# Performance work log

Measured on AMD Instinct MI355X. Metric: run time of the kernel, lower is better.

## Reference

```python
import jax, jax.numpy as jnp
import numpy as np

C, G = 512, 16            # channels, groups
GC = C // G               # group channels = 32
OFFSET_SCALE = 1.0
EPS = 1e-6


def setup_inputs() -> dict:
    key = jax.random.key(0)
    ks = jax.random.split(key, 4)
    N, H, W = 8, 64, 64
    return {
        "input_first": jax.random.normal(ks[0], (N, C, H, W), jnp.float32),
        "input_last": jax.random.normal(ks[1], (N, H, W, C), jnp.float32),
        "dw_w": jax.random.normal(ks[2], (C, 1, 3, 3), jnp.float32) * 0.1,  # depthwise kernel (OIHW, I=1)
        "dw_b": jnp.zeros((C,), jnp.float32),
        "ln_g": jnp.ones((C,), jnp.float32),
        "ln_b": jnp.zeros((C,), jnp.float32),
        "off_w": jax.random.normal(ks[3], (2 * G, C), jnp.float32) * 0.02,  # nonzero (module zero-inits)
        "off_b": jnp.zeros((2 * G,), jnp.float32),
    }


def _bilinear(img, px, py):
    # align_corners=False, padding_mode='zeros'.
    Hin, Win, _ = img.shape
    x0 = jnp.floor(px)
    y0 = jnp.floor(py)
    wx1 = px - x0
    wy1 = py - y0

    def tap(xi, yi, w):
        xc = jnp.clip(xi, 0, Win - 1).astype(jnp.int32)
        yc = jnp.clip(yi, 0, Hin - 1).astype(jnp.int32)
        valid = ((xi >= 0) & (xi <= Win - 1) & (yi >= 0) & (yi <= Hin - 1)).astype(img.dtype)
        return img[yc, xc] * (w * valid)[:, None]  # [L, GC]

    return (tap(x0, y0, (1 - wx1) * (1 - wy1)) + tap(x0 + 1, y0, wx1 * (1 - wy1)) +
            tap(x0, y0 + 1, (1 - wx1) * wy1) + tap(x0 + 1, y0 + 1, wx1 * wy1))


_sampler = jax.vmap(jax.vmap(_bilinear))  # over [N, G, ...]


def _forward(input_first, input_last, dw_w, dw_b, ln_g, ln_b, off_w, off_b):
    N, _, H, W = input_first.shape
    # --- dw_conv: depthwise 3x3 conv (pad 1) -> LN (channels_last) -> GELU ---
    x = jax.lax.conv_general_dilated(
        input_first, dw_w, window_strides=(1, 1), padding='SAME',
        dimension_numbers=('NCHW', 'OIHW', 'NCHW'), feature_group_count=C)
    x = x + dw_b[None, :, None, None]
    x = jnp.transpose(x, (0, 2, 3, 1))  # NHWC
    mu = x.mean(-1, keepdims=True)
    var = x.var(-1, keepdims=True)
    x1 = (x - mu) * jax.lax.rsqrt(var + EPS) * ln_g + ln_b
    x1 = jax.nn.gelu(x1, approximate=False)

    # --- offset prediction: [N,H,W, G*2], pairs are (x, y) per DCNv3 layout ---
    off = jnp.einsum('nhwc,oc->nhwo', x1, off_w) + off_b
    off = off.reshape(N, H, W, G, 2)

    # --- DCNv3 core, kernel_size=1, pad=0, stride=1, dilation=1 ---
    # ref point = pixel center; normalized loc = (i+0.5)/size + off*scale/size;
    # grid_sample pixel coord = loc*size - 0.5 = i + off*scale.
    px = jnp.arange(W, dtype=x1.dtype)[None, None, :, None] + off[..., 0] * OFFSET_SCALE  # [N,H,W,G]
    py = jnp.arange(H, dtype=x1.dtype)[None, :, None, None] + off[..., 1] * OFFSET_SCALE
    px = px.transpose(0, 3, 1, 2).reshape(N, G, H * W)
    py = py.transpose(0, 3, 1, 2).reshape(N, G, H * W)

    img = input_last.reshape(N, H, W, G, GC).transpose(0, 3, 1, 2, 4)  # [N,G,H,W,GC]
    sampled = _sampler(img, px, py)  # [N,G,HW,GC]

    mask = jnp.ones((N, G, H * W, 1), dtype=input_last.dtype)  # mask_dcn = ones
    out = (sampled * mask).reshape(N, G, H, W, GC)
    out = out.transpose(0, 2, 3, 1, 4).reshape(N, H, W, C)
    return jnp.transpose(out, (0, 3, 1, 2))  # NCHW, as in module's final permute


def reference(input_first, input_last, dw_w, dw_b, ln_g, ln_b, off_w, off_b):
    return _forward(input_first, input_last, dw_w, dw_b, ln_g, ln_b, off_w, off_b)
```

## Files before the change

### kernel.cpp

```cpp
#include <hip/hip_runtime.h>
#include <hip/hip_bf16.h>
#include <math.h>

#define NB 8
#define CC 512
#define HH 64
#define WW 64
#define GG 16
#define GCH 32
#define OO 32
#define NGHW (NB * GG * HH * WW)
#define NPX  (NB * HH * WW)


__device__ __forceinline__ float gelu_exact(float x) {
    return 0.5f * x * (1.0f + erff(x * 0.70710678118654752f));
}

__device__ __forceinline__ unsigned pack_bf2(float a, float b) {
    __hip_bfloat162 t = __float22bfloat162_rn(make_float2(a, b));
    return *(unsigned*)&t;
}

__global__ __launch_bounds__(512, 2)
void conv_ln_gelu_kernel(const float* __restrict__ in_first,
                         const float* __restrict__ dw_w,
                         const float* __restrict__ dw_b,
                         const float* __restrict__ ln_g,
                         const float* __restrict__ ln_b,
                         __hip_bfloat16* __restrict__ x1)
{
    const int h   = blockIdx.x;
    const int n   = blockIdx.y;
    const int tid = threadIdx.x;
    const int wq   = tid & 15;
    const int cgrp = tid >> 4;
    const int wb = wq * 4;
    const int c0 = cgrp * 16;

    __shared__ float redS [64 * 33];
    __shared__ float redS2[64 * 33];
    __shared__ float meanArr[64];
    __shared__ float rstdArr[64];

    float xv[4][16];
    float sw [4] = {0.f, 0.f, 0.f, 0.f};
    float sw2[4] = {0.f, 0.f, 0.f, 0.f};

    #pragma unroll
    for (int i = 0; i < 16; ++i) {
        const int c = c0 + i;
        float w9[9];
        #pragma unroll
        for (int k = 0; k < 9; ++k) w9[k] = dw_w[c * 9 + k];
        const float b = dw_b[c];
        float a0 = b, a1 = b, a2 = b, a3 = b;
        #pragma unroll
        for (int r = 0; r < 3; ++r) {
            const int y = h + r - 1;
            if (y < 0 || y >= HH) continue;
            const float* rowp = in_first + ((n * CC + c) * HH + y) * WW;
            const float4 m = *(const float4*)(rowp + wb);
            float left  = __shfl_up(m.w, 1);
            float right = __shfl_down(m.x, 1);
            if (wq == 0)  left  = 0.0f;
            if (wq == 15) right = 0.0f;
            const float k0 = w9[r * 3 + 0], k1 = w9[r * 3 + 1], k2 = w9[r * 3 + 2];
            a0 += k0 * left + k1 * m.x + k2 * m.y;
            a1 += k0 * m.x  + k1 * m.y + k2 * m.z;
            a2 += k0 * m.y  + k1 * m.z + k2 * m.w;
            a3 += k0 * m.z  + k1 * m.w + k2 * right;
        }
        xv[0][i] = a0; xv[1][i] = a1; xv[2][i] = a2; xv[3][i] = a3;
        sw[0] += a0; sw2[0] += a0 * a0;
        sw[1] += a1; sw2[1] += a1 * a1;
        sw[2] += a2; sw2[2] += a2 * a2;
        sw[3] += a3; sw2[3] += a3 * a3;
    }

    #pragma unroll
    for (int j = 0; j < 4; ++j) {
        redS [(wb + j) * 33 + cgrp] = sw[j];
        redS2[(wb + j) * 33 + cgrp] = sw2[j];
    }
    __syncthreads();
    if (tid < 64) {
        const int w = tid;
        float s = 0.f, s2 = 0.f;
        for (int k = 0; k < 32; ++k) {
            s  += redS [w * 33 + k];
            s2 += redS2[w * 33 + k];
        }
        const float mu  = s * (1.0f / 512.0f);
        const float var = s2 * (1.0f / 512.0f) - mu * mu;
        meanArr[w] = mu;
        rstdArr[w] = rsqrtf(var + 1e-6f);
    }
    __syncthreads();

    float mu_[4], rs_[4];
    #pragma unroll
    for (int j = 0; j < 4; ++j) { mu_[j] = meanArr[wb + j]; rs_[j] = rstdArr[wb + j]; }
    #pragma unroll
    for (int i = 0; i < 16; ++i) {
        const int c = c0 + i;
        const float lg = ln_g[c];
        const float lb = ln_b[c];
        #pragma unroll
        for (int j = 0; j < 4; ++j) {
            const float v = (xv[j][i] - mu_[j]) * rs_[j] * lg + lb;
            xv[j][i] = gelu_exact(v);
        }
    }
    const int rowbase = (n * HH + h) * WW;
    #pragma unroll
    for (int j = 0; j < 4; ++j) {
        unsigned up[8];
        #pragma unroll
        for (int t = 0; t < 8; ++t) up[t] = pack_bf2(xv[j][2 * t], xv[j][2 * t + 1]);
        uint4* dst = (uint4*)(x1 + ((size_t)(rowbase + wb + j) * CC + c0));
        dst[0] = make_uint4(up[0], up[1], up[2], up[3]);
        dst[1] = make_uint4(up[4], up[5], up[6], up[7]);
    }
}

typedef __attribute__((ext_vector_type(8))) short bf16x8;
typedef __attribute__((ext_vector_type(4))) float f32x4;

__global__ __launch_bounds__(256)
void offmat_kernel(const __hip_bfloat16* __restrict__ x1,
                   const float* __restrict__ off_w,
                   const float* __restrict__ off_b,
                   float* __restrict__ coords)
{
    const int tid  = threadIdx.x;
    const int wave = tid >> 6;
    const int lane = tid & 63;
    const int m0   = (blockIdx.x * 4 + wave) * 16;
    const int ml   = lane & 15;
    const int quad = lane >> 4;

    f32x4 acc0 = {0.f, 0.f, 0.f, 0.f};
    f32x4 acc1 = {0.f, 0.f, 0.f, 0.f};

    const short* arow  = (const short*)x1 + (size_t)(m0 + ml) * CC + quad * 8;
    const float* b0row = off_w + (size_t)ml * CC + quad * 8;
    const float* b1row = off_w + (size_t)(ml + 16) * CC + quad * 8;

    for (int k = 0; k < CC; k += 32) {
        const bf16x8 af = *(const bf16x8*)(arow + k);

        const float4 p0 = *(const float4*)(b0row + k);
        const float4 q0 = *(const float4*)(b0row + k + 4);
        union { bf16x8 v; unsigned u[4]; } b0;
        b0.u[0] = pack_bf2(p0.x, p0.y); b0.u[1] = pack_bf2(p0.z, p0.w);
        b0.u[2] = pack_bf2(q0.x, q0.y); b0.u[3] = pack_bf2(q0.z, q0.w);
        acc0 = __builtin_amdgcn_mfma_f32_16x16x32_bf16(af, b0.v, acc0, 0, 0, 0);

        const float4 p1 = *(const float4*)(b1row + k);
        const float4 q1 = *(const float4*)(b1row + k + 4);
        union { bf16x8 v; unsigned u[4]; } b1;
        b1.u[0] = pack_bf2(p1.x, p1.y); b1.u[1] = pack_bf2(p1.z, p1.w);
        b1.u[2] = pack_bf2(q1.x, q1.y); b1.u[3] = pack_bf2(q1.z, q1.w);
        acc1 = __builtin_amdgcn_mfma_f32_16x16x32_bf16(af, b1.v, acc1, 0, 0, 0);
    }

    const int   o0  = ml;
    const int   o1  = ml + 16;
    const float ob0 = off_b[o0];
    const float ob1 = off_b[o1];
    const int   par = o0 & 1;
    const int   g0  = o0 >> 1;
    const int   g1  = o1 >> 1;

    #pragma unroll
    for (int r = 0; r < 4; ++r) {
        const int m  = m0 + quad * 4 + r;
        const int w  = m & 63;
        const int hh = (m >> 6) & 63;
        const int nn = m >> 12;
        const float base = par ? (float)hh : (float)w;
        coords[(size_t)par * NGHW + (((size_t)nn * GG + g0) * HH + hh) * WW + w]
            = base + acc0[r] + ob0;
        coords[(size_t)par * NGHW + (((size_t)nn * GG + g1) * HH + hh) * WW + w]
            = base + acc1[r] + ob1;
    }
}

__global__ __launch_bounds__(256)
void sample_kernel(const float* __restrict__ in_last,
                   const float* __restrict__ coord_ws,
                   float* __restrict__ out)
{
    const int h   = blockIdx.x;
    const int n   = blockIdx.y;
    const int g   = blockIdx.z;
    const int tid = threadIdx.x;

    __shared__ float pxs[64];
    __shared__ float pys[64];
    __shared__ float smem[64 * 33];

    if (tid < 128) {
        const int w = tid & 63;
        const size_t cidx = (((size_t)n * GG + g) * HH + h) * WW + w;
        if (tid < 64) pxs[w] = coord_ws[cidx];
        else          pys[w] = coord_ws[cidx + NGHW];
    }
    __syncthreads();

    const int c4    = tid & 7;
    const int wslot = tid >> 3;
    const float* base = in_last + (size_t)n * HH * WW * CC + g * GCH + c4 * 4;

    #pragma unroll
    for (int pass = 0; pass < 2; ++pass) {
        const int w = wslot + pass * 32;
        const float px = pxs[w];
        const float py = pys[w];
        const float x0f = floorf(px), y0f = floorf(py);
        const float fx = px - x0f, fy = py - y0f;
        const int x0 = (int)x0f, y0 = (int)y0f;

        float4 acc = make_float4(0.f, 0.f, 0.f, 0.f);
        #pragma unroll
        for (int t = 0; t < 4; ++t) {
            const int xi = x0 + (t & 1);
            const int yi = y0 + (t >> 1);
            const float wt = ((t & 1) ? fx : 1.0f - fx) * ((t >> 1) ? fy : 1.0f - fy);
            if (xi >= 0 && xi < WW && yi >= 0 && yi < HH) {
                const float4 v = *(const float4*)(base + ((size_t)yi * WW + xi) * CC);
                acc.x += wt * v.x;
                acc.y += wt * v.y;
                acc.z += wt * v.z;
                acc.w += wt * v.w;
            }
        }
        float* sp = smem + w * 33 + c4 * 4;
        sp[0] = acc.x; sp[1] = acc.y; sp[2] = acc.z; sp[3] = acc.w;
    }
    __syncthreads();

    const int w  = tid & 63;
    const int cb = tid >> 6;
    float* op = out + (((size_t)n * CC + g * GCH) * HH + h) * WW + w;
    #pragma unroll
    for (int pass = 0; pass < 8; ++pass) {
        const int c = pass * 4 + cb;
        op[(size_t)c * (HH * WW)] = smem[w * 33 + c];
    }
}

extern "C" void kernel_launch(void* const* d_in, const int* in_sizes, int n_in,
                              void* d_out, int out_size, void* d_ws, size_t ws_size,
                              hipStream_t stream) {
    const float* in_first = (const float*)d_in[0];
    const float* in_last  = (const float*)d_in[1];
    const float* dw_w     = (const float*)d_in[2];
    const float* dw_b     = (const float*)d_in[3];
    const float* ln_g     = (const float*)d_in[4];
    const float* ln_b     = (const float*)d_in[5];
    const float* off_w    = (const float*)d_in[6];
    const float* off_b    = (const float*)d_in[7];
    float* out = (float*)d_out;

    float*          coord_ws = (float*)d_ws;
    __hip_bfloat16* x1       = (__hip_bfloat16*)((char*)d_ws + (size_t)4 * 1024 * 1024);

    dim3 gridA(HH, NB);
    conv_ln_gelu_kernel<<<gridA, 512, 0, stream>>>(in_first, dw_w, dw_b, ln_g, ln_b, x1);

    offmat_kernel<<<NPX / 64, 256, 0, stream>>>(x1, off_w, off_b, coord_ws);

    dim3 gridB(HH, NB, GG);
    sample_kernel<<<gridB, 256, 0, stream>>>(in_last, coord_ws, out);
}
```

Measured before the change: 295.9 us.

## Fuse depthwise conv/LN/GELU with offset matmul via LDS staging

Merges the conv+LayerNorm+GELU kernel and the offset-projection MFMA kernel into one 1024-thread block per image row. The GELU output is packed to bf16 in a padded shared-memory buffer and consumed directly by 8 waves doing MFMA, removing the global x1 round trip and one launch. The thread mapping changes to 2 pixels per thread and the LN reduction now uses a cross-half shuffle. In exchange only 8 of 16 waves do the matmul, the large LDS footprint may limit occupancy, and each block reloads off_w.

```diff
diff --git a/kernel.cpp b/kernel.cpp
--- a/kernel.cpp
+++ b/kernel.cpp
@@ -11,6 +11,7 @@
 #define OO 32
 #define NGHW (NB * GG * HH * WW)
 #define NPX  (NB * HH * WW)
+#define XROW 520
 
 
 __device__ __forceinline__ float gelu_exact(float x) {
@@ -22,30 +23,39 @@
     return *(unsigned*)&t;
 }
 
-__global__ __launch_bounds__(512, 2)
-void conv_ln_gelu_kernel(const float* __restrict__ in_first,
-                         const float* __restrict__ dw_w,
-                         const float* __restrict__ dw_b,
-                         const float* __restrict__ ln_g,
-                         const float* __restrict__ ln_b,
-                         __hip_bfloat16* __restrict__ x1)
+typedef __attribute__((ext_vector_type(8))) short bf16x8;
+typedef __attribute__((ext_vector_type(4))) float f32x4;
+
+__global__ __launch_bounds__(1024, 4)
+void fused_conv_ln_gelu_off_kernel(const float* __restrict__ in_first,
+                                   const float* __restrict__ dw_w,
+                                   const float* __restrict__ dw_b,
+                                   const float* __restrict__ ln_g,
+                                   const float* __restrict__ ln_b,
+                                   const float* __restrict__ off_w,
+                                   const float* __restrict__ off_b,
+                                   float* __restrict__ coords)
 {
-    const int h   = blockIdx.x;
-    const int n   = blockIdx.y;
-    const int tid = threadIdx.x;
-    const int wq   = tid & 15;
-    const int cgrp = tid >> 4;
-    const int wb = wq * 4;
-    const int c0 = cgrp * 16;
-
-    __shared__ float redS [64 * 33];
-    __shared__ float redS2[64 * 33];
-    __shared__ float meanArr[64];
-    __shared__ float rstdArr[64];
-
-    float xv[4][16];
-    float sw [4] = {0.f, 0.f, 0.f, 0.f};
-    float sw2[4] = {0.f, 0.f, 0.f, 0.f};
+    const int h    = blockIdx.x;
+    const int n    = blockIdx.y;
+    const int tid  = threadIdx.x;
+    const int wq   = tid & 31;
+    const int cgrp = tid >> 5;
+    const int wb   = wq * 2;
+    const int c0   = cgrp * 16;
+    const int wave = tid >> 6;
+    const int lane = tid & 63;
+
+    __shared__ short xbuf[64 * XROW];
+    __shared__ float redS [16 * 64];
+    __shared__ float redS2[16 * 64];
+    __shared__ float mu_s[64];
+    __shared__ float rs_s[64];
+
+    float xv[2][16];
+    float sw0 = 0.f, sw1 = 0.f, sq0 = 0.f, sq1 = 0.f;
+
+    const float* inbase = in_first + (size_t)(n * CC + c0) * HH * WW;
 
     #pragma unroll
     for (int i = 0; i < 16; ++i) {
@@ -54,136 +64,102 @@
         #pragma unroll
         for (int k = 0; k < 9; ++k) w9[k] = dw_w[c * 9 + k];
         const float b = dw_b[c];
-        float a0 = b, a1 = b, a2 = b, a3 = b;
+        float a0 = b, a1 = b;
         #pragma unroll
         for (int r = 0; r < 3; ++r) {
             const int y = h + r - 1;
             if (y < 0 || y >= HH) continue;
-            const float* rowp = in_first + ((n * CC + c) * HH + y) * WW;
-            const float4 m = *(const float4*)(rowp + wb);
-            float left  = __shfl_up(m.w, 1);
+            const float2 m = *(const float2*)(inbase + ((size_t)i * HH + y) * WW + wb);
+            float left  = __shfl_up(m.y, 1);
             float right = __shfl_down(m.x, 1);
             if (wq == 0)  left  = 0.0f;
-            if (wq == 15) right = 0.0f;
+            if (wq == 31) right = 0.0f;
             const float k0 = w9[r * 3 + 0], k1 = w9[r * 3 + 1], k2 = w9[r * 3 + 2];
             a0 += k0 * left + k1 * m.x + k2 * m.y;
-            a1 += k0 * m.x  + k1 * m.y + k2 * m.z;
-            a2 += k0 * m.y  + k1 * m.z + k2 * m.w;
-            a3 += k0 * m.z  + k1 * m.w + k2 * right;
-        }
-        xv[0][i] = a0; xv[1][i] = a1; xv[2][i] = a2; xv[3][i] = a3;
-        sw[0] += a0; sw2[0] += a0 * a0;
-        sw[1] += a1; sw2[1] += a1 * a1;
-        sw[2] += a2; sw2[2] += a2 * a2;
-        sw[3] += a3; sw2[3] += a3 * a3;
-    }
-
-    #pragma unroll
-    for (int j = 0; j < 4; ++j) {
-        redS [(wb + j) * 33 + cgrp] = sw[j];
-        redS2[(wb + j) * 33 + cgrp] = sw2[j];
+            a1 += k0 * m.x  + k1 * m.y + k2 * right;
+        }
+        xv[0][i] = a0; xv[1][i] = a1;
+        sw0 += a0; sq0 += a0 * a0;
+        sw1 += a1; sq1 += a1 * a1;
+    }
+
+    sw0 += __shfl_xor(sw0, 32); sq0 += __shfl_xor(sq0, 32);
+    sw1 += __shfl_xor(sw1, 32); sq1 += __shfl_xor(sq1, 32);
+    if (lane < 32) {
+        redS [wave * 64 + wb + 0] = sw0;  redS2[wave * 64 + wb + 0] = sq0;
+        redS [wave * 64 + wb + 1] = sw1;  redS2[wave * 64 + wb + 1] = sq1;
     }
     __syncthreads();
     if (tid < 64) {
-        const int w = tid;
         float s = 0.f, s2 = 0.f;
-        for (int k = 0; k < 32; ++k) {
-            s  += redS [w * 33 + k];
-            s2 += redS2[w * 33 + k];
+        #pragma unroll
+        for (int k = 0; k < 16; ++k) {
+            s  += redS [k * 64 + tid];
+            s2 += redS2[k * 64 + tid];
         }
         const float mu  = s * (1.0f / 512.0f);
         const float var = s2 * (1.0f / 512.0f) - mu * mu;
-        meanArr[w] = mu;
-        rstdArr[w] = rsqrtf(var + 1e-6f);
-    }
-    __syncthreads();
-
-    float mu_[4], rs_[4];
-    #pragma unroll
-    for (int j = 0; j < 4; ++j) { mu_[j] = meanArr[wb + j]; rs_[j] = rstdArr[wb + j]; }
-    #pragma unroll
-    for (int i = 0; i < 16; ++i) {
-        const int c = c0 + i;
-        const float lg = ln_g[c];
-        const float lb = ln_b[c];
-        #pragma unroll
-        for (int j = 0; j < 4; ++j) {
-            const float v = (xv[j][i] - mu_[j]) * rs_[j] * lg + lb;
-            xv[j][i] = gelu_exact(v);
-        }
-    }
-    const int rowbase = (n * HH + h) * WW;
-    #pragma unroll
-    for (int j = 0; j < 4; ++j) {
-        unsigned up[8];
-        #pragma unroll
-        for (int t = 0; t < 8; ++t) up[t] = pack_bf2(xv[j][2 * t], xv[j][2 * t + 1]);
-        uint4* dst = (uint4*)(x1 + ((size_t)(rowbase + wb + j) * CC + c0));
-        dst[0] = make_uint4(up[0], up[1], up[2], up[3]);
-        dst[1] = make_uint4(up[4], up[5], up[6], up[7]);
-    }
-}
-
-typedef __attribute__((ext_vector_type(8))) short bf16x8;
-typedef __attribute__((ext_vector_type(4))) float f32x4;
-
-__global__ __launch_bounds__(256)
-void offmat_kernel(const __hip_bfloat16* __restrict__ x1,
-                   const float* __restrict__ off_w,
-                   const float* __restrict__ off_b,
-                   float* __restrict__ coords)
-{
-    const int tid  = threadIdx.x;
-    const int wave = tid >> 6;
-    const int lane = tid & 63;
-    const int m0   = (blockIdx.x * 4 + wave) * 16;
-    const int ml   = lane & 15;
-    const int quad = lane >> 4;
-
-    f32x4 acc0 = {0.f, 0.f, 0.f, 0.f};
-    f32x4 acc1 = {0.f, 0.f, 0.f, 0.f};
-
-    const short* arow  = (const short*)x1 + (size_t)(m0 + ml) * CC + quad * 8;
-    const float* b0row = off_w + (size_t)ml * CC + quad * 8;
-    const float* b1row = off_w + (size_t)(ml + 16) * CC + quad * 8;
-
-    for (int k = 0; k < CC; k += 32) {
-        const bf16x8 af = *(const bf16x8*)(arow + k);
-
-        const float4 p0 = *(const float4*)(b0row + k);
-        const float4 q0 = *(const float4*)(b0row + k + 4);
-        union { bf16x8 v; unsigned u[4]; } b0;
-        b0.u[0] = pack_bf2(p0.x, p0.y); b0.u[1] = pack_bf2(p0.z, p0.w);
-        b0.u[2] = pack_bf2(q0.x, q0.y); b0.u[3] = pack_bf2(q0.z, q0.w);
-        acc0 = __builtin_amdgcn_mfma_f32_16x16x32_bf16(af, b0.v, acc0, 0, 0, 0);
-
-        const float4 p1 = *(const float4*)(b1row + k);
-        const float4 q1 = *(const float4*)(b1row + k + 4);
-        union { bf16x8 v; unsigned u[4]; } b1;
-        b1.u[0] = pack_bf2(p1.x, p1.y); b1.u[1] = pack_bf2(p1.z, p1.w);
-        b1.u[2] = pack_bf2(q1.x, q1.y); b1.u[3] = pack_bf2(q1.z, q1.w);
-        acc1 = __builtin_amdgcn_mfma_f32_16x16x32_bf16(af, b1.v, acc1, 0, 0, 0);
-    }
-
-    const int   o0  = ml;
-    const int   o1  = ml + 16;
-    const float ob0 = off_b[o0];
-    const float ob1 = off_b[o1];
-    const int   par = o0 & 1;
-    const int   g0  = o0 >> 1;
-    const int   g1  = o1 >> 1;
-
-    #pragma unroll
-    for (int r = 0; r < 4; ++r) {
-        const int m  = m0 + quad * 4 + r;
-        const int w  = m & 63;
-        const int hh = (m >> 6) & 63;
-        const int nn = m >> 12;
-        const float base = par ? (float)hh : (float)w;
-        coords[(size_t)par * NGHW + (((size_t)nn * GG + g0) * HH + hh) * WW + w]
-            = base + acc0[r] + ob0;
-        coords[(size_t)par * NGHW + (((size_t)nn * GG + g1) * HH + hh) * WW + w]
-            = base + acc1[r] + ob1;
+        mu_s[tid] = mu;
+        rs_s[tid] = rsqrtf(var + 1e-6f);
+    }
+    __syncthreads();
+
+    {
+        const float mu0 = mu_s[wb + 0], rs0 = rs_s[wb + 0];
+        const float mu1 = mu_s[wb + 1], rs1 = rs_s[wb + 1];
+        unsigned pk0[8], pk1[8];
+        #pragma unroll
+        for (int t = 0; t < 8; ++t) {
+            const int c = c0 + 2 * t;
+            const float lgA = ln_g[c],     lbA = ln_b[c];
+            const float lgB = ln_g[c + 1], lbB = ln_b[c + 1];
+            const float v0a = (xv[0][2 * t]     - mu0) * rs0 * lgA + lbA;
+            const float v0b = (xv[0][2 * t + 1] - mu0) * rs0 * lgB + lbB;
+            const float v1a = (xv[1][2 * t]     - mu1) * rs1 * lgA + lbA;
+            const float v1b = (xv[1][2 * t + 1] - mu1) * rs1 * lgB + lbB;
+            pk0[t] = pack_bf2(gelu_exact(v0a), gelu_exact(v0b));
+            pk1[t] = pack_bf2(gelu_exact(v1a), gelu_exact(v1b));
+        }
+        short* p0 = xbuf + (wb + 0) * XROW + c0;
+        short* p1 = xbuf + (wb + 1) * XROW + c0;
+        *(uint4*)(p0)     = make_uint4(pk0[0], pk0[1], pk0[2], pk0[3]);
+        *(uint4*)(p0 + 8) = make_uint4(pk0[4], pk0[5], pk0[6], pk0[7]);
+        *(uint4*)(p1)     = make_uint4(pk1[0], pk1[1], pk1[2], pk1[3]);
+        *(uint4*)(p1 + 8) = make_uint4(pk1[4], pk1[5], pk1[6], pk1[7]);
+    }
+    __syncthreads();
+
+    if (wave < 8) {
+        const int ml   = lane & 15;
+        const int quad = lane >> 4;
+        const int pxT  = wave >> 1;
+        const int oT   = wave & 1;
+
+        const short* arow = xbuf + (pxT * 16 + ml) * XROW + quad * 8;
+        const float* brow = off_w + (size_t)(oT * 16 + ml) * CC + quad * 8;
+
+        f32x4 acc = {0.f, 0.f, 0.f, 0.f};
+        for (int k = 0; k < CC; k += 32) {
+            const bf16x8 af = *(const bf16x8*)(arow + k);
+            const float4 p = *(const float4*)(brow + k);
+            const float4 q = *(const float4*)(brow + k + 4);
+            union { bf16x8 v; unsigned u[4]; } bb;
+            bb.u[0] = pack_bf2(p.x, p.y); bb.u[1] = pack_bf2(p.z, p.w);
+            bb.u[2] = pack_bf2(q.x, q.y); bb.u[3] = pack_bf2(q.z, q.w);
+            acc = __builtin_amdgcn_mfma_f32_16x16x32_bf16(af, bb.v, acc, 0, 0, 0);
+        }
+
+        const int   o   = oT * 16 + ml;
+        const float ob  = off_b[o];
+        const int   par = o & 1;
+        const int   g   = o >> 1;
+        #pragma unroll
+        for (int r = 0; r < 4; ++r) {
+            const int w = pxT * 16 + quad * 4 + r;
+            const float base = par ? (float)h : (float)w;
+            coords[(size_t)par * NGHW + (((size_t)n * GG + g) * HH + h) * WW + w]
+                = base + acc[r] + ob;
+        }
     }
 }
 
@@ -264,13 +240,11 @@
     const float* off_b    = (const float*)d_in[7];
     float* out = (float*)d_out;
 
-    float*          coord_ws = (float*)d_ws;
-    __hip_bfloat16* x1       = (__hip_bfloat16*)((char*)d_ws + (size_t)4 * 1024 * 1024);
+    float* coord_ws = (float*)d_ws;
 
     dim3 gridA(HH, NB);
-    conv_ln_gelu_kernel<<<gridA, 512, 0, stream>>>(in_first, dw_w, dw_b, ln_g, ln_b, x1);
-
-    offmat_kernel<<<NPX / 64, 256, 0, stream>>>(x1, off_w, off_b, coord_ws);
+    fused_conv_ln_gelu_off_kernel<<<gridA, 1024, 0, stream>>>(
+        in_first, dw_w, dw_b, ln_g, ln_b, off_w, off_b, coord_ws);
 
     dim3 gridB(HH, NB, GG);
     sample_kernel<<<gridB, 256, 0, stream>>>(in_last, coord_ws, out);
```

Result: faster. 282.7 us (-4.4%).
